# Kernel optimization log

Measured on AMD Instinct MI355X. Metric: run time of the kernel, lower is better.

Reference implementation:

```python
import jax, jax.numpy as jnp
import numpy as np

N_NODES = 100000
N_EDGES = 1000000
NODE_DIM = 64
HIDDEN_DIM = 128


def setup_inputs() -> dict:
    key = jax.random.key(0)
    ks = jax.random.split(key, 9)
    x = jax.random.normal(ks[0], (N_NODES, NODE_DIM), dtype=jnp.float32)
    y = jax.random.normal(ks[1], (N_NODES, NODE_DIM), dtype=jnp.float32)
    edge_index = jax.random.randint(ks[2], (2, N_EDGES), 0, N_NODES, dtype=jnp.int64)
    pos_x = jax.random.normal(ks[3], (N_NODES, 3), dtype=jnp.float32)
    pos_y = jax.random.normal(ks[4], (N_NODES, 3), dtype=jnp.float32)
    in_dim = NODE_DIM * 2 + 1
    # Kaiming-uniform-ish init like torch Linear
    lim1 = 1.0 / np.sqrt(in_dim)
    lim2 = 1.0 / np.sqrt(HIDDEN_DIM)
    W1 = jax.random.uniform(ks[5], (in_dim, HIDDEN_DIM), jnp.float32, -lim1, lim1)
    b1 = jax.random.uniform(ks[6], (HIDDEN_DIM,), jnp.float32, -lim1, lim1)
    W2 = jax.random.uniform(ks[7], (HIDDEN_DIM, 1), jnp.float32, -lim2, lim2)
    b2 = jax.random.uniform(ks[8], (1,), jnp.float32, -lim2, lim2)
    return {"x": x, "y": y, "edge_index": edge_index, "pos_x": pos_x,
            "pos_y": pos_y, "W1": W1, "b1": b1, "W2": W2, "b2": b2}


def reference(x, y, edge_index, pos_x, pos_y, W1, b1, W2, b2):
    src = edge_index[0]
    dst = edge_index[1]
    # per-edge euclidean distance between endpoint positions  [E]
    d = pos_x[src] - pos_y[dst]                      # [E, 3]
    dist = jnp.sqrt(jnp.sum(d * d, axis=1))          # [E]
    # gather + concat: [E, node_dim*2 + 1]
    mlp_in = jnp.concatenate([x[src], y[dst], dist[:, None]], axis=1)
    h = jax.nn.relu(mlp_in @ W1 + b1)                # [E, hidden]
    out = jax.nn.relu(h @ W2 + b2)                   # [E, 1]
    return out
```

## Files before the change

kernel.cpp:

```cpp
#include <hip/hip_runtime.h>
#include <hip/hip_bf16.h>


constexpr int NDIM  = 64;
constexpr int HID   = 128;
constexpr int KPAD  = 136;

typedef __attribute__((ext_vector_type(8))) short  short8;
typedef __attribute__((ext_vector_type(4))) int    int4v;
typedef __attribute__((ext_vector_type(4))) float  floatx4;

__device__ __forceinline__ short f2bf(float f) {
    union { __hip_bfloat16 h; short s; } cv;
    cv.h = __float2bfloat16(f);
    return cv.s;
}

__device__ __forceinline__ int pack2(float a, float b) {
    union { __hip_bfloat162 h; int u; } cv;
    cv.h = __float22bfloat162_rn(float2{a, b});
    return cv.u;
}

__device__ __forceinline__ short8 make_afrag_f32(const float* rp) {
    const floatx4 f0 = *reinterpret_cast<const floatx4*>(rp);
    const floatx4 f1 = *reinterpret_cast<const floatx4*>(rp + 4);
    union { int4v i; short8 s8; } cv;
    cv.i.x = pack2(f0.x, f0.y);
    cv.i.y = pack2(f0.z, f0.w);
    cv.i.z = pack2(f1.x, f1.y);
    cv.i.w = pack2(f1.z, f1.w);
    return cv.s8;
}

__global__ __launch_bounds__(256) void cvt_kernel(
    const float* __restrict__ xin, const float* __restrict__ yin,
    short* __restrict__ xb, short* __restrict__ yb, int nfl)
{
    const int stride = gridDim.x * blockDim.x;
    const int n8 = nfl >> 3;
    for (int i = blockIdx.x * blockDim.x + threadIdx.x; i < n8; i += stride) {
        {
            const floatx4 f0 = *reinterpret_cast<const floatx4*>(xin + i * 8);
            const floatx4 f1 = *reinterpret_cast<const floatx4*>(xin + i * 8 + 4);
            union { int4v v; short8 s; } c;
            c.v.x = pack2(f0.x, f0.y); c.v.y = pack2(f0.z, f0.w);
            c.v.z = pack2(f1.x, f1.y); c.v.w = pack2(f1.z, f1.w);
            *reinterpret_cast<short8*>(xb + i * 8) = c.s;
        }
        {
            const floatx4 f0 = *reinterpret_cast<const floatx4*>(yin + i * 8);
            const floatx4 f1 = *reinterpret_cast<const floatx4*>(yin + i * 8 + 4);
            union { int4v v; short8 s; } c;
            c.v.x = pack2(f0.x, f0.y); c.v.y = pack2(f0.z, f0.w);
            c.v.z = pack2(f1.x, f1.y); c.v.w = pack2(f1.z, f1.w);
            *reinterpret_cast<short8*>(yb + i * 8) = c.s;
        }
    }
}

template <bool BF16GATHER>
__global__ __launch_bounds__(256, 3) void edge_mlp_kernel(
    const float* __restrict__ x, const float* __restrict__ y,
    const short* __restrict__ xb, const short* __restrict__ yb,
    const int*  __restrict__ ei, const float* __restrict__ px,
    const float* __restrict__ py, const float* __restrict__ W1,
    const float* __restrict__ b1, const float* __restrict__ W2,
    const float* __restrict__ b2, float* __restrict__ out, int E)
{
    __shared__ __align__(16) short Wt[HID * KPAD];

    const int tid = threadIdx.x;

    for (int base = 0; base < HID * HID; base += 256 * 8) {
        float f[8];
#pragma unroll
        for (int u = 0; u < 8; ++u) f[u] = W1[base + u * 256 + tid];
#pragma unroll
        for (int u = 0; u < 8; ++u) {
            int i = base + u * 256 + tid;
            Wt[(i & 127) * KPAD + (i >> 7)] = f2bf(f[u]);
        }
    }
    if (tid < HID) {
        const int n = tid;
        Wt[n * KPAD + 128] = f2bf(W1[128 * HID + n]);
        Wt[n * KPAD + 129] = f2bf(b1[n]);
#pragma unroll
        for (int j = 130; j < 136; ++j) Wt[n * KPAD + j] = 0;
    }
    __syncthreads();

    const int lane = tid & 63;
    const int wave = tid >> 6;
    const int quad = lane >> 4;
    const int lm   = lane & 15;

    float w2v[8];
#pragma unroll
    for (int t = 0; t < 8; ++t) w2v[t] = W2[t * 16 + lm];
    const float b2s = b2[0];

    const int* __restrict__ srcp = ei;
    const int* __restrict__ dstp = ei + E;

    const int sel5 = (quad == 0) ? 128 : 0;

    const int ntiles = (E + 127) / 128;
    for (int tile = blockIdx.x; tile < ntiles; tile += gridDim.x) {
        const int mb = tile * 128 + wave * 32;
        int m0 = mb + lm;       if (m0 >= E) m0 = E - 1;
        int m1 = mb + 16 + lm;  if (m1 >= E) m1 = E - 1;
        const int src0 = srcp[m0], dst0 = dstp[m0];
        const int src1 = srcp[m1], dst1 = dstp[m1];

        const float dx0 = px[src0 * 3 + 0] - py[dst0 * 3 + 0];
        const float dy0 = px[src0 * 3 + 1] - py[dst0 * 3 + 1];
        const float dz0 = px[src0 * 3 + 2] - py[dst0 * 3 + 2];
        const float dist0 = sqrtf(dx0 * dx0 + dy0 * dy0 + dz0 * dz0);
        const float dx1 = px[src1 * 3 + 0] - py[dst1 * 3 + 0];
        const float dy1 = px[src1 * 3 + 1] - py[dst1 * 3 + 1];
        const float dz1 = px[src1 * 3 + 2] - py[dst1 * 3 + 2];
        const float dist1 = sqrtf(dx1 * dx1 + dy1 * dy1 + dz1 * dz1);

        short8 fa[4], fb[4];
#pragma unroll
        for (int s = 0; s < 4; ++s) {
            const int kk = s * 32 + quad * 8;
            if (BF16GATHER) {
                const short* pa = (s < 2) ? (xb + src0 * NDIM + kk)
                                          : (yb + dst0 * NDIM + (kk - 64));
                const short* pb = (s < 2) ? (xb + src1 * NDIM + kk)
                                          : (yb + dst1 * NDIM + (kk - 64));
                fa[s] = *reinterpret_cast<const short8*>(pa);
                fb[s] = *reinterpret_cast<const short8*>(pb);
            } else {
                fa[s] = make_afrag_f32((s < 2) ? (x + src0 * NDIM + kk)
                                               : (y + dst0 * NDIM + (kk - 64)));
                fb[s] = make_afrag_f32((s < 2) ? (x + src1 * NDIM + kk)
                                               : (y + dst1 * NDIM + (kk - 64)));
            }
        }
        short8 fa4, fb4;
        {
            union { int4v i; short8 s8; } ca, cb;
            const int d0 = (quad == 0) ? pack2(dist0, 1.0f) : 0;
            const int d1 = (quad == 0) ? pack2(dist1, 1.0f) : 0;
            ca.i = int4v{d0, 0, 0, 0};
            cb.i = int4v{d1, 0, 0, 0};
            fa4 = ca.s8; fb4 = cb.s8;
        }

        floatx4 accA[8], accB[8];
#pragma unroll
        for (int t = 0; t < 8; ++t) {
            accA[t] = floatx4{0.f, 0.f, 0.f, 0.f};
            accB[t] = floatx4{0.f, 0.f, 0.f, 0.f};
        }

        int zoff = 0;
        asm volatile("" : "+v"(zoff));
        const short* wr  = Wt + zoff + lm * KPAD + quad * 8;
        const short* wr5 = Wt + zoff + lm * KPAD + sel5;

#pragma unroll
        for (int t = 0; t < 8; ++t) {
            const short* base = wr + t * (16 * KPAD);
            const short8 bg0 = *reinterpret_cast<const short8*>(base);
            const short8 bg1 = *reinterpret_cast<const short8*>(base + 32);
            const short8 bg2 = *reinterpret_cast<const short8*>(base + 64);
            const short8 bg3 = *reinterpret_cast<const short8*>(base + 96);
            const short8 bg4 = *reinterpret_cast<const short8*>(wr5 + t * (16 * KPAD));
            accA[t] = __builtin_amdgcn_mfma_f32_16x16x32_bf16(fa[0], bg0, accA[t], 0, 0, 0);
            accB[t] = __builtin_amdgcn_mfma_f32_16x16x32_bf16(fb[0], bg0, accB[t], 0, 0, 0);
            accA[t] = __builtin_amdgcn_mfma_f32_16x16x32_bf16(fa[1], bg1, accA[t], 0, 0, 0);
            accB[t] = __builtin_amdgcn_mfma_f32_16x16x32_bf16(fb[1], bg1, accB[t], 0, 0, 0);
            accA[t] = __builtin_amdgcn_mfma_f32_16x16x32_bf16(fa[2], bg2, accA[t], 0, 0, 0);
            accB[t] = __builtin_amdgcn_mfma_f32_16x16x32_bf16(fb[2], bg2, accB[t], 0, 0, 0);
            accA[t] = __builtin_amdgcn_mfma_f32_16x16x32_bf16(fa[3], bg3, accA[t], 0, 0, 0);
            accB[t] = __builtin_amdgcn_mfma_f32_16x16x32_bf16(fb[3], bg3, accB[t], 0, 0, 0);
            accA[t] = __builtin_amdgcn_mfma_f32_16x16x32_bf16(fa4,  bg4, accA[t], 0, 0, 0);
            accB[t] = __builtin_amdgcn_mfma_f32_16x16x32_bf16(fb4,  bg4, accB[t], 0, 0, 0);
        }

        float p0 = 0.f, p1 = 0.f, p2 = 0.f, p3 = 0.f;
        float q0 = 0.f, q1 = 0.f, q2 = 0.f, q3 = 0.f;
#pragma unroll
        for (int t = 0; t < 8; ++t) {
            p0 += fmaxf(accA[t][0], 0.f) * w2v[t];
            p1 += fmaxf(accA[t][1], 0.f) * w2v[t];
            p2 += fmaxf(accA[t][2], 0.f) * w2v[t];
            p3 += fmaxf(accA[t][3], 0.f) * w2v[t];
            q0 += fmaxf(accB[t][0], 0.f) * w2v[t];
            q1 += fmaxf(accB[t][1], 0.f) * w2v[t];
            q2 += fmaxf(accB[t][2], 0.f) * w2v[t];
            q3 += fmaxf(accB[t][3], 0.f) * w2v[t];
        }
#pragma unroll
        for (int off = 1; off < 16; off <<= 1) {
            p0 += __shfl_xor(p0, off, 64);
            p1 += __shfl_xor(p1, off, 64);
            p2 += __shfl_xor(p2, off, 64);
            p3 += __shfl_xor(p3, off, 64);
            q0 += __shfl_xor(q0, off, 64);
            q1 += __shfl_xor(q1, off, 64);
            q2 += __shfl_xor(q2, off, 64);
            q3 += __shfl_xor(q3, off, 64);
        }
        if (lm < 4) {
            const float vA = (lm == 0) ? p0 : (lm == 1) ? p1 : (lm == 2) ? p2 : p3;
            const float vB = (lm == 0) ? q0 : (lm == 1) ? q1 : (lm == 2) ? q2 : q3;
            const int eA = mb + quad * 4 + lm;
            const int eB = mb + 16 + quad * 4 + lm;
            if (eA < E) out[eA] = fmaxf(vA + b2s, 0.f);
            if (eB < E) out[eB] = fmaxf(vB + b2s, 0.f);
        }
    }
}

extern "C" void kernel_launch(void* const* d_in, const int* in_sizes, int n_in,
                              void* d_out, int out_size, void* d_ws, size_t ws_size,
                              hipStream_t stream)
{
    const float* x  = (const float*)d_in[0];
    const float* y  = (const float*)d_in[1];
    const int*   ei = (const int*)  d_in[2];
    const float* px = (const float*)d_in[3];
    const float* py = (const float*)d_in[4];
    const float* W1 = (const float*)d_in[5];
    const float* b1 = (const float*)d_in[6];
    const float* W2 = (const float*)d_in[7];
    const float* b2 = (const float*)d_in[8];
    float* out = (float*)d_out;
    const int E = in_sizes[2] / 2;
    const int nnode_elems = in_sizes[0];

    const size_t need = (size_t)nnode_elems * 2 * sizeof(short);
    if (ws_size >= need) {
        short* xb = (short*)d_ws;
        short* yb = xb + nnode_elems;
        cvt_kernel<<<dim3(1024), dim3(256), 0, stream>>>(x, y, xb, yb, nnode_elems);
        edge_mlp_kernel<true><<<dim3(768), dim3(256), 0, stream>>>(
            x, y, xb, yb, ei, px, py, W1, b1, W2, b2, out, E);
    } else {
        edge_mlp_kernel<false><<<dim3(768), dim3(256), 0, stream>>>(
            x, y, nullptr, nullptr, ei, px, py, W1, b1, W2, b2, out, E);
    }
}
```

Baseline: 162.6 us.

## Precompute edge distances in convert kernel and prefetch next tile indices

The convert kernel now also computes each edge's distance and stores it in the workspace as bf16, so the main kernel no longer gathers pos_x/pos_y per tile. The main kernel software-pipelines the edge-index and distance loads, fetching the next tile's indices during the current tile's work. Occupancy is raised from 3 to 4 blocks per SM, and the grid grows from 768 to 1024 blocks. In exchange the prep kernel gains a random gather pass over a million edges and an extra bf16 array write, plus more register pressure from the prefetched values.

```diff
diff --git a/kernel.cpp b/kernel.cpp
--- a/kernel.cpp
+++ b/kernel.cpp
@@ -35,11 +35,15 @@
 
 __global__ __launch_bounds__(256) void cvt_kernel(
     const float* __restrict__ xin, const float* __restrict__ yin,
-    short* __restrict__ xb, short* __restrict__ yb, int nfl)
+    const int*  __restrict__ ei,  const float* __restrict__ px,
+    const float* __restrict__ py,
+    short* __restrict__ xb, short* __restrict__ yb, short* __restrict__ db,
+    int nfl, int E)
 {
     const int stride = gridDim.x * blockDim.x;
+    const int gid = blockIdx.x * blockDim.x + threadIdx.x;
     const int n8 = nfl >> 3;
-    for (int i = blockIdx.x * blockDim.x + threadIdx.x; i < n8; i += stride) {
+    for (int i = gid; i < n8; i += stride) {
         {
             const floatx4 f0 = *reinterpret_cast<const floatx4*>(xin + i * 8);
             const floatx4 f1 = *reinterpret_cast<const floatx4*>(xin + i * 8 + 4);
@@ -57,12 +61,21 @@
             *reinterpret_cast<short8*>(yb + i * 8) = c.s;
         }
     }
+    for (int e = gid; e < E; e += stride) {
+        const int s = ei[e];
+        const int d = ei[E + e];
+        const float dx = px[s * 3 + 0] - py[d * 3 + 0];
+        const float dy = px[s * 3 + 1] - py[d * 3 + 1];
+        const float dz = px[s * 3 + 2] - py[d * 3 + 2];
+        db[e] = f2bf(sqrtf(dx * dx + dy * dy + dz * dz));
+    }
 }
 
 template <bool BF16GATHER>
-__global__ __launch_bounds__(256, 3) void edge_mlp_kernel(
+__global__ __launch_bounds__(256, 4) void edge_mlp_kernel(
     const float* __restrict__ x, const float* __restrict__ y,
     const short* __restrict__ xb, const short* __restrict__ yb,
+    const short* __restrict__ db,
     const int*  __restrict__ ei, const float* __restrict__ px,
     const float* __restrict__ py, const float* __restrict__ W1,
     const float* __restrict__ b1, const float* __restrict__ W2,
@@ -107,21 +120,48 @@
     const int sel5 = (quad == 0) ? 128 : 0;
 
     const int ntiles = (E + 127) / 128;
-    for (int tile = blockIdx.x; tile < ntiles; tile += gridDim.x) {
+    int tile = blockIdx.x;
+    if (tile >= ntiles) return;
+
+    int s0, d0, s1, d1;
+    short dd0 = 0, dd1 = 0;
+    float fd0 = 0.f, fd1 = 0.f;
+    {
         const int mb = tile * 128 + wave * 32;
-        int m0 = mb + lm;       if (m0 >= E) m0 = E - 1;
-        int m1 = mb + 16 + lm;  if (m1 >= E) m1 = E - 1;
-        const int src0 = srcp[m0], dst0 = dstp[m0];
-        const int src1 = srcp[m1], dst1 = dstp[m1];
-
-        const float dx0 = px[src0 * 3 + 0] - py[dst0 * 3 + 0];
-        const float dy0 = px[src0 * 3 + 1] - py[dst0 * 3 + 1];
-        const float dz0 = px[src0 * 3 + 2] - py[dst0 * 3 + 2];
-        const float dist0 = sqrtf(dx0 * dx0 + dy0 * dy0 + dz0 * dz0);
-        const float dx1 = px[src1 * 3 + 0] - py[dst1 * 3 + 0];
-        const float dy1 = px[src1 * 3 + 1] - py[dst1 * 3 + 1];
-        const float dz1 = px[src1 * 3 + 2] - py[dst1 * 3 + 2];
-        const float dist1 = sqrtf(dx1 * dx1 + dy1 * dy1 + dz1 * dz1);
+        const int m0 = min(mb + lm, E - 1);
+        const int m1 = min(mb + 16 + lm, E - 1);
+        s0 = srcp[m0]; d0 = dstp[m0]; s1 = srcp[m1]; d1 = dstp[m1];
+        if (BF16GATHER) {
+            if (quad == 0) { dd0 = db[m0]; dd1 = db[m1]; }
+        }
+    }
+
+    for (; tile < ntiles; tile += gridDim.x) {
+        const int nt = tile + gridDim.x;
+        const int qt = (nt < ntiles) ? nt : tile;
+        const int qmb = qt * 128 + wave * 32;
+        const int qm0 = min(qmb + lm, E - 1);
+        const int qm1 = min(qmb + 16 + lm, E - 1);
+        const int ns0 = srcp[qm0], nd0 = dstp[qm0];
+        const int ns1 = srcp[qm1], nd1 = dstp[qm1];
+        short ndd0 = 0, ndd1 = 0;
+        if (BF16GATHER) {
+            if (quad == 0) { ndd0 = db[qm0]; ndd1 = db[qm1]; }
+        }
+
+        const int mb = tile * 128 + wave * 32;
+        const int src0 = s0, dst0 = d0, src1 = s1, dst1 = d1;
+
+        if (!BF16GATHER) {
+            const float dx0 = px[src0 * 3 + 0] - py[dst0 * 3 + 0];
+            const float dy0 = px[src0 * 3 + 1] - py[dst0 * 3 + 1];
+            const float dz0 = px[src0 * 3 + 2] - py[dst0 * 3 + 2];
+            fd0 = sqrtf(dx0 * dx0 + dy0 * dy0 + dz0 * dz0);
+            const float dx1 = px[src1 * 3 + 0] - py[dst1 * 3 + 0];
+            const float dy1 = px[src1 * 3 + 1] - py[dst1 * 3 + 1];
+            const float dz1 = px[src1 * 3 + 2] - py[dst1 * 3 + 2];
+            fd1 = sqrtf(dx1 * dx1 + dy1 * dy1 + dz1 * dz1);
+        }
 
         short8 fa[4], fb[4];
 #pragma unroll
@@ -144,10 +184,16 @@
         short8 fa4, fb4;
         {
             union { int4v i; short8 s8; } ca, cb;
-            const int d0 = (quad == 0) ? pack2(dist0, 1.0f) : 0;
-            const int d1 = (quad == 0) ? pack2(dist1, 1.0f) : 0;
-            ca.i = int4v{d0, 0, 0, 0};
-            cb.i = int4v{d1, 0, 0, 0};
+            int p0i, p1i;
+            if (BF16GATHER) {
+                p0i = (quad == 0) ? (0x3F800000 | (int)(unsigned short)dd0) : 0;
+                p1i = (quad == 0) ? (0x3F800000 | (int)(unsigned short)dd1) : 0;
+            } else {
+                p0i = (quad == 0) ? pack2(fd0, 1.0f) : 0;
+                p1i = (quad == 0) ? pack2(fd1, 1.0f) : 0;
+            }
+            ca.i = int4v{p0i, 0, 0, 0};
+            cb.i = int4v{p1i, 0, 0, 0};
             fa4 = ca.s8; fb4 = cb.s8;
         }
 
@@ -215,6 +261,9 @@
             if (eA < E) out[eA] = fmaxf(vA + b2s, 0.f);
             if (eB < E) out[eB] = fmaxf(vB + b2s, 0.f);
         }
+
+        s0 = ns0; d0 = nd0; s1 = ns1; d1 = nd1;
+        dd0 = ndd0; dd1 = ndd1;
     }
 }
 
@@ -235,15 +284,18 @@
     const int E = in_sizes[2] / 2;
     const int nnode_elems = in_sizes[0];
 
-    const size_t need = (size_t)nnode_elems * 2 * sizeof(short);
+    const size_t need = (size_t)nnode_elems * 2 * sizeof(short)
+                      + (size_t)E * sizeof(short);
     if (ws_size >= need) {
         short* xb = (short*)d_ws;
         short* yb = xb + nnode_elems;
-        cvt_kernel<<<dim3(1024), dim3(256), 0, stream>>>(x, y, xb, yb, nnode_elems);
-        edge_mlp_kernel<true><<<dim3(768), dim3(256), 0, stream>>>(
-            x, y, xb, yb, ei, px, py, W1, b1, W2, b2, out, E);
+        short* db = yb + nnode_elems;
+        cvt_kernel<<<dim3(1024), dim3(256), 0, stream>>>(
+            x, y, ei, px, py, xb, yb, db, nnode_elems, E);
+        edge_mlp_kernel<true><<<dim3(1024), dim3(256), 0, stream>>>(
+            x, y, xb, yb, db, ei, px, py, W1, b1, W2, b2, out, E);
     } else {
-        edge_mlp_kernel<false><<<dim3(768), dim3(256), 0, stream>>>(
-            x, y, nullptr, nullptr, ei, px, py, W1, b1, W2, b2, out, E);
-    }
-}
+        edge_mlp_kernel<false><<<dim3(1024), dim3(256), 0, stream>>>(
+            x, y, nullptr, nullptr, nullptr, ei, px, py, W1, b1, W2, b2, out, E);
+    }
+}
```

Result: no change. 165.0 us (+1.5%).
